# Optimization experiments

Hardware: AMD Instinct MI355X
Metric: run time of the kernel (lower is better)

Reference implementation:

```python
import jax, jax.numpy as jnp
import numpy as np

B, T_IN, F, H = 256, 168, 128, 512
T_OUT = 48


def setup_inputs() -> dict:
    key = jax.random.key(0)
    ks = jax.random.split(key, 8)
    s = 1.0 / np.sqrt(H)
    return {
        "x": jax.random.normal(ks[0], (B, T_IN, F), dtype=jnp.float32),
        "enc_Wih": jax.random.normal(ks[1], (4 * H, F), dtype=jnp.float32) * s,
        "enc_Whh": jax.random.normal(ks[2], (4 * H, H), dtype=jnp.float32) * s,
        "enc_b": jax.random.normal(ks[3], (4 * H,), dtype=jnp.float32) * s,
        "dec_Wih": jax.random.normal(ks[4], (4 * H, F), dtype=jnp.float32) * s,
        "dec_Whh": jax.random.normal(ks[5], (4 * H, H), dtype=jnp.float32) * s,
        "dec_b": jax.random.normal(ks[6], (4 * H,), dtype=jnp.float32) * s,
        "W_lin": jax.random.normal(ks[7], (F, H), dtype=jnp.float32) * s,
        "t_out": T_OUT,
    }


def _lstm_cell(h, c, xt, Wih, Whh, b):
    # torch gate order: i, f, g, o
    gates = xt @ Wih.T + h @ Whh.T + b  # [B, 4H]
    i, f, g, o = jnp.split(gates, 4, axis=-1)
    c_new = jax.nn.sigmoid(f) * c + jax.nn.sigmoid(i) * jnp.tanh(g)
    h_new = jax.nn.sigmoid(o) * jnp.tanh(c_new)
    return h_new, c_new


def reference(x, enc_Wih, enc_Whh, enc_b, dec_Wih, dec_Whh, dec_b, W_lin, t_out):
    bsz = x.shape[0]
    hidden = enc_Whh.shape[1]
    h0 = jnp.zeros((bsz, hidden), x.dtype)
    c0 = jnp.zeros((bsz, hidden), x.dtype)

    # ---- encoder: scan over T_in ----
    def enc_step(carry, xt):
        h, c = carry
        h, c = _lstm_cell(h, c, xt, enc_Wih, enc_Whh, enc_b)
        return (h, c), None

    (hn, cn), _ = jax.lax.scan(enc_step, (h0, c0), jnp.swapaxes(x, 0, 1))

    # ---- decoder: recursive feeding, scan over T_out ----
    dec_in0 = x[:, -1, :]  # [B, F]

    def dec_step(carry, _):
        h, c, inp = carry
        h, c = _lstm_cell(h, c, inp, dec_Wih, dec_Whh, dec_b)
        out = h @ W_lin.T  # [B, F]
        return (h, c, out), out

    _, outs = jax.lax.scan(dec_step, (hn, cn, dec_in0), None, length=t_out)
    return jnp.swapaxes(outs, 0, 1)  # [B, T_out, F]
```

## Files before the change

kernel.cpp:

```cpp
#include <hip/hip_runtime.h>
#include <hip/hip_bf16.h>

typedef __bf16 bf16_t;
typedef __bf16 bf16x8 __attribute__((ext_vector_type(8)));
typedef __bf16 bf16x4 __attribute__((ext_vector_type(4)));
typedef float  f32x4  __attribute__((ext_vector_type(4)));
typedef unsigned int u32;
typedef unsigned long long u64;

#define HID 512
#define BATCH 256
#define TIN 168
#define TOUT 48
#define FEAT 128
#define NSTEPS (TIN + TOUT)
#define NGRP 8
#define NJT 32
#define GRPB 32

__device__ __forceinline__ float sigmoidf_(float x) {
    x = fminf(fmaxf(x, -30.f), 30.f);
    return 1.f / (1.f + __expf(-x));
}
__device__ __forceinline__ float tanhf_(float x) {
    x = fminf(fmaxf(x, -15.f), 15.f);
    float e = __expf(2.f * x);
    return (e - 1.f) / (e + 1.f);
}

__device__ __forceinline__ bf16x8 ld_h8(const bf16_t* p) {
    union { u64 q[2]; bf16x8 v; } u;
    u.q[0] = __hip_atomic_load((const u64*)p,     __ATOMIC_RELAXED,
                               __HIP_MEMORY_SCOPE_SYSTEM);
    u.q[1] = __hip_atomic_load((const u64*)p + 1, __ATOMIC_RELAXED,
                               __HIP_MEMORY_SCOPE_SYSTEM);
    return u.v;
}
__device__ __forceinline__ void st_h4(bf16_t* p, float v0, float v1, float v2, float v3) {
    bf16_t b0 = (bf16_t)v0, b1 = (bf16_t)v1, b2 = (bf16_t)v2, b3 = (bf16_t)v3;
    unsigned short s0, s1, s2, s3;
    __builtin_memcpy(&s0, &b0, 2); __builtin_memcpy(&s1, &b1, 2);
    __builtin_memcpy(&s2, &b2, 2); __builtin_memcpy(&s3, &b3, 2);
    u64 w = (u64)s0 | ((u64)s1 << 16) | ((u64)s2 << 32) | ((u64)s3 << 48);
    __hip_atomic_store((u64*)p, w, __ATOMIC_RELAXED, __HIP_MEMORY_SCOPE_SYSTEM);
}

__global__ __launch_bounds__(256)
void cast_x_kernel(const float* __restrict__ x, bf16_t* __restrict__ Xbf) {
    int q = blockIdx.x * 256 + threadIdx.x;
    if (q >= BATCH * TIN * (FEAT / 4)) return;
    int f4  = q & 31;
    int rem = q >> 5;
    int t = rem % TIN;
    int b = rem / TIN;
    float4 v = *(const float4*)&x[((size_t)b * TIN + t) * FEAT + f4 * 4];
    bf16x4 o = { (bf16_t)v.x, (bf16_t)v.y, (bf16_t)v.z, (bf16_t)v.w };
    *(bf16x4*)&Xbf[((size_t)t * BATCH + b) * FEAT + f4 * 4] = o;
}

__global__ __launch_bounds__(256)
void cast_wcat_kernel(const float* __restrict__ Wih, const float* __restrict__ Whh,
                      bf16_t* __restrict__ Wcat) {
    int q = blockIdx.x * 256 + threadIdx.x;
    int k4 = q % 160;
    int r  = q / 160;
    if (r >= 2048) return;
    int k = k4 * 4;
    float4 v;
    if (k < FEAT) v = *(const float4*)&Wih[(size_t)r * FEAT + k];
    else          v = *(const float4*)&Whh[(size_t)r * HID + (k - FEAT)];
    bf16x4 o = { (bf16_t)v.x, (bf16_t)v.y, (bf16_t)v.z, (bf16_t)v.w };
    *(bf16x4*)&Wcat[(size_t)r * 640 + k] = o;
}

__global__ __launch_bounds__(256)
void cast_wlin_kernel(const float* __restrict__ W, bf16_t* __restrict__ Wb) {
    int q = blockIdx.x * 256 + threadIdx.x;
    if (q >= FEAT * HID / 4) return;
    float4 v = *(const float4*)&W[q * 4];
    bf16x4 o = { (bf16_t)v.x, (bf16_t)v.y, (bf16_t)v.z, (bf16_t)v.w };
    *(bf16x4*)&Wb[q * 4] = o;
}

__global__ __launch_bounds__(256)
void build_wcomb_kernel(const float* __restrict__ dWih, const float* __restrict__ dWhh,
                        const float* __restrict__ Wlin, bf16_t* __restrict__ Wcomb) {
    __shared__ float As[64][128];
    __shared__ float Bs[128][64];
    int r0 = blockIdx.x * 64, c0 = blockIdx.y * 64;
    int tid = threadIdx.x;
    for (int i = tid; i < 64 * 32; i += 256) {
        int rr = i >> 5, cc = (i & 31) << 2;
        *(float4*)&As[rr][cc] = *(const float4*)&dWih[(size_t)(r0 + rr) * 128 + cc];
    }
    for (int i = tid; i < 128 * 16; i += 256) {
        int kk = i >> 4, cc = (i & 15) << 2;
        *(float4*)&Bs[kk][cc] = *(const float4*)&Wlin[(size_t)kk * HID + c0 + cc];
    }
    __syncthreads();
    int tx = tid & 15, ty = tid >> 4;
    float acc[4][4] = {};
    for (int k = 0; k < 128; ++k) {
        float a[4], b[4];
        #pragma unroll
        for (int i = 0; i < 4; ++i) a[i] = As[ty * 4 + i][k];
        #pragma unroll
        for (int j = 0; j < 4; ++j) b[j] = Bs[k][tx * 4 + j];
        #pragma unroll
        for (int i = 0; i < 4; ++i)
            #pragma unroll
            for (int j = 0; j < 4; ++j) acc[i][j] += a[i] * b[j];
    }
    for (int i = 0; i < 4; ++i) {
        int r = r0 + ty * 4 + i;
        for (int j = 0; j < 4; ++j) {
            int cc = c0 + tx * 4 + j;
            Wcomb[(size_t)r * HID + cc] = (bf16_t)(acc[i][j] + dWhh[(size_t)r * HID + cc]);
        }
    }
}


__device__ __forceinline__ void group_wait(const u32* flags, int g, int tid,
                                           unsigned int epoch) {
    if (tid < NJT) {
        while (__hip_atomic_load(&flags[g * NJT + tid], __ATOMIC_RELAXED,
                                 __HIP_MEMORY_SCOPE_SYSTEM) < epoch)
            __builtin_amdgcn_s_sleep(1);
    }
    __syncthreads();
}

__device__ __forceinline__ void group_arrive(u32* flags, int g, int jt, int tid,
                                             unsigned int epoch) {
    if (tid == 0)
        __hip_atomic_store(&flags[g * NJT + jt], epoch, __ATOMIC_RELAXED,
                           __HIP_MEMORY_SCOPE_SYSTEM);
}

__device__ __forceinline__ void cell_finish(
    f32x4 (&acc)[4], float (&cacc)[4], f32x4 (*Ex)[2][64],
    int gp, int bh, int lane, int l15, int l4, int brow, int jq0,
    bf16_t* __restrict__ hnext)
{
    if (gp == 1) {
        #pragma unroll
        for (int q = 0; q < 4; ++q)
            Ex[q][bh][lane] = acc[q];
    }
    __syncthreads();
    if (gp == 0) {
        #pragma unroll
        for (int q = 0; q < 4; ++q)
            acc[q] += Ex[q][bh][lane];
        float hv[4];
        #pragma unroll
        for (int r = 0; r < 4; ++r) {
            float cn = sigmoidf_(acc[1][r]) * cacc[r] + sigmoidf_(acc[0][r]) * tanhf_(acc[2][r]);
            cacc[r] = cn;
            hv[r] = sigmoidf_(acc[3][r]) * tanhf_(cn);
        }
        st_h4(hnext + (size_t)brow * HID + jq0, hv[0], hv[1], hv[2], hv[3]);
        asm volatile("s_waitcnt vmcnt(0)" ::: "memory");
    }
    __syncthreads();
}

__global__ __launch_bounds__(256, 1)
void lstm_persist(const bf16_t* __restrict__ Xbf,
                  const bf16_t* __restrict__ Wenc, const float* __restrict__ enc_b,
                  const bf16_t* __restrict__ Wdec1, const bf16_t* __restrict__ Wcomb,
                  const float* __restrict__ dec_b,
                  bf16_t* __restrict__ hbufA, bf16_t* __restrict__ hbufB,
                  bf16_t* __restrict__ Hdec, u32* __restrict__ flags)
{
    __shared__ f32x4 Ex[4][2][64];
    const int bid = blockIdx.x;
    const int g   = bid & (NGRP - 1);
    const int jt  = bid >> 3;
    const int j0  = jt * 16;
    const int tid = threadIdx.x;
    const int wave = tid >> 6, lane = tid & 63;
    const int l15 = lane & 15, l4 = lane >> 4;
    const int bh = wave & 1, gp = wave >> 1;
    const int b0 = g * GRPB + bh * 16;
    const int arow = b0 + l15;
    const int jcol = j0 + l15;
    const int jq0  = j0 + l4 * 4;

    f32x4 biasE4[4], biasD4[4];
    #pragma unroll
    for (int q = 0; q < 4; ++q) {
        biasE4[q] = *(const f32x4*)&enc_b[q * HID + jq0];
        biasD4[q] = *(const f32x4*)&dec_b[q * HID + jq0];
    }
    float cacc[4] = {0.f, 0.f, 0.f, 0.f};

    bf16x8 Breg[40];
    const int kc0 = gp * 320;

    #pragma unroll
    for (int q = 0; q < 4; ++q)
        #pragma unroll
        for (int i = 0; i < 10; ++i)
            Breg[q * 10 + i] = *(const bf16x8*)(
                Wenc + (size_t)(q * HID + jcol) * 640 + kc0 + i * 32 + l4 * 8);
    #pragma unroll
    for (int n = 0; n < 40; ++n) asm volatile("" : "+v"(Breg[n]));

    for (int t = 0; t < TIN; ++t) {
        if (t > 0) group_wait(flags, g, tid, (unsigned)t);
        const bf16_t* hb = (t & 1) ? hbufB : hbufA;
        bf16_t* hn       = (t & 1) ? hbufA : hbufB;
        const bf16_t* xb  = Xbf + ((size_t)t * BATCH + arow) * FEAT + l4 * 8;
        const bf16_t* hbp = hb + (size_t)arow * HID + l4 * 8;
        bf16x8 a[10];
        if (gp == 0) {
            #pragma unroll
            for (int i = 0; i < 4; ++i)  a[i] = *(const bf16x8*)(xb + i * 32);
            #pragma unroll
            for (int i = 4; i < 10; ++i) a[i] = ld_h8(hbp + (i * 32 - FEAT));
        } else {
            #pragma unroll
            for (int i = 0; i < 10; ++i) a[i] = ld_h8(hbp + (320 - FEAT) + i * 32);
        }
        f32x4 acc[4];
        #pragma unroll
        for (int q = 0; q < 4; ++q)
            acc[q] = (gp == 0) ? biasE4[q] : (f32x4){0.f, 0.f, 0.f, 0.f};
        #pragma unroll
        for (int i = 0; i < 10; ++i)
            #pragma unroll
            for (int q = 0; q < 4; ++q)
                acc[q] = __builtin_amdgcn_mfma_f32_16x16x32_bf16(Breg[q * 10 + i], a[i], acc[q], 0, 0, 0);
        cell_finish(acc, cacc, Ex, gp, bh, lane, l15, l4, arow, jq0, hn);
        group_arrive(flags, g, jt, tid, (unsigned)(t + 1));
    }

    #pragma unroll
    for (int q = 0; q < 4; ++q)
        #pragma unroll
        for (int i = 0; i < 10; ++i)
            Breg[q * 10 + i] = *(const bf16x8*)(
                Wdec1 + (size_t)(q * HID + jcol) * 640 + kc0 + i * 32 + l4 * 8);
    #pragma unroll
    for (int n = 0; n < 40; ++n) asm volatile("" : "+v"(Breg[n]));

    {
        const int t = TIN;
        group_wait(flags, g, tid, (unsigned)t);
        const bf16_t* xb  = Xbf + ((size_t)(TIN - 1) * BATCH + arow) * FEAT + l4 * 8;
        const bf16_t* hbp = hbufA + (size_t)arow * HID + l4 * 8;
        bf16x8 a[10];
        if (gp == 0) {
            #pragma unroll
            for (int i = 0; i < 4; ++i)  a[i] = *(const bf16x8*)(xb + i * 32);
            #pragma unroll
            for (int i = 4; i < 10; ++i) a[i] = ld_h8(hbp + (i * 32 - FEAT));
        } else {
            #pragma unroll
            for (int i = 0; i < 10; ++i) a[i] = ld_h8(hbp + (320 - FEAT) + i * 32);
        }
        f32x4 acc[4];
        #pragma unroll
        for (int q = 0; q < 4; ++q)
            acc[q] = (gp == 0) ? biasD4[q] : (f32x4){0.f, 0.f, 0.f, 0.f};
        #pragma unroll
        for (int i = 0; i < 10; ++i)
            #pragma unroll
            for (int q = 0; q < 4; ++q)
                acc[q] = __builtin_amdgcn_mfma_f32_16x16x32_bf16(Breg[q * 10 + i], a[i], acc[q], 0, 0, 0);
        cell_finish(acc, cacc, Ex, gp, bh, lane, l15, l4, arow, jq0, Hdec);
        group_arrive(flags, g, jt, tid, (unsigned)(t + 1));
    }

    const int kd0 = gp * 256;
    #pragma unroll
    for (int q = 0; q < 4; ++q)
        #pragma unroll
        for (int i = 0; i < 8; ++i)
            Breg[q * 8 + i] = *(const bf16x8*)(
                Wcomb + (size_t)(q * HID + jcol) * HID + kd0 + i * 32 + l4 * 8);
    #pragma unroll
    for (int n = 0; n < 32; ++n) asm volatile("" : "+v"(Breg[n]));

    for (int t = TIN + 1; t < NSTEPS; ++t) {
        group_wait(flags, g, tid, (unsigned)t);
        const bf16_t* hprev = Hdec + (size_t)(t - 1 - TIN) * BATCH * HID
                                   + (size_t)arow * HID + l4 * 8;
        bf16x8 a[8];
        #pragma unroll
        for (int i = 0; i < 8; ++i)
            a[i] = ld_h8(hprev + kd0 + i * 32);
        f32x4 acc[4];
        #pragma unroll
        for (int q = 0; q < 4; ++q)
            acc[q] = (gp == 0) ? biasD4[q] : (f32x4){0.f, 0.f, 0.f, 0.f};
        #pragma unroll
        for (int i = 0; i < 8; ++i)
            #pragma unroll
            for (int q = 0; q < 4; ++q)
                acc[q] = __builtin_amdgcn_mfma_f32_16x16x32_bf16(Breg[q * 8 + i], a[i], acc[q], 0, 0, 0);
        cell_finish(acc, cacc, Ex, gp, bh, lane, l15, l4, arow, jq0,
                    Hdec + (size_t)(t - TIN) * BATCH * HID);
        group_arrive(flags, g, jt, tid, (unsigned)(t + 1));
    }
}

__global__ __launch_bounds__(128)
void final_proj_kernel(const bf16_t* __restrict__ Hdec, const bf16_t* __restrict__ Wlin,
                       float* __restrict__ out) {
    int tid = threadIdx.x;
    int wv = tid >> 6, lane = tid & 63;
    int l15 = lane & 15, l4 = lane >> 4;
    int row0 = blockIdx.x * 32 + wv * 16;
    const bf16_t* arow = Hdec + (size_t)(row0 + l15) * HID;
    f32x4 acc[8];
    #pragma unroll
    for (int n = 0; n < 8; ++n) acc[n] = (f32x4){0.f, 0.f, 0.f, 0.f};
    #pragma unroll 4
    for (int kc = 0; kc < HID; kc += 32) {
        bf16x8 af = *(const bf16x8*)(arow + kc + l4 * 8);
        #pragma unroll
        for (int n = 0; n < 8; ++n) {
            bf16x8 bfr = *(const bf16x8*)(Wlin + (size_t)(n * 16 + l15) * HID + kc + l4 * 8);
            acc[n] = __builtin_amdgcn_mfma_f32_16x16x32_bf16(af, bfr, acc[n], 0, 0, 0);
        }
    }
    #pragma unroll
    for (int n = 0; n < 8; ++n) {
        int f = n * 16 + l15;
        #pragma unroll
        for (int r = 0; r < 4; ++r) {
            int row = row0 + l4 * 4 + r;
            int t = row >> 8;
            int b = row & 255;
            out[(size_t)b * (TOUT * FEAT) + (size_t)t * FEAT + f] = acc[n][r];
        }
    }
}

extern "C" void kernel_launch(void* const* d_in, const int* in_sizes, int n_in,
                              void* d_out, int out_size, void* d_ws, size_t ws_size,
                              hipStream_t stream) {
    const float* x       = (const float*)d_in[0];
    const float* enc_Wih = (const float*)d_in[1];
    const float* enc_Whh = (const float*)d_in[2];
    const float* enc_b   = (const float*)d_in[3];
    const float* dec_Wih = (const float*)d_in[4];
    const float* dec_Whh = (const float*)d_in[5];
    const float* dec_b   = (const float*)d_in[6];
    const float* W_lin   = (const float*)d_in[7];
    float* out = (float*)d_out;

    char* p = (char*)d_ws;
    auto alloc = [&](size_t bytes) -> void* {
        void* r = (void*)p;
        p += (bytes + 255) & ~(size_t)255;
        return r;
    };
    bf16_t* Xbf    = (bf16_t*)alloc((size_t)TIN * BATCH * FEAT * 2);
    bf16_t* Wenc   = (bf16_t*)alloc((size_t)2048 * 640 * 2);
    bf16_t* Wdec1  = (bf16_t*)alloc((size_t)2048 * 640 * 2);
    bf16_t* Wcomb  = (bf16_t*)alloc((size_t)2048 * HID * 2);
    bf16_t* Wlinb  = (bf16_t*)alloc((size_t)FEAT * HID * 2);
    bf16_t* hbufA  = (bf16_t*)alloc((size_t)BATCH * HID * 2);
    bf16_t* hbufB  = (bf16_t*)alloc((size_t)BATCH * HID * 2);
    bf16_t* Hdec   = (bf16_t*)alloc((size_t)TOUT * BATCH * HID * 2);
    u32* flags     = (u32*)alloc((size_t)NGRP * NJT * 4);

    (void)hipMemsetAsync(hbufA, 0, (size_t)BATCH * HID * 2, stream);
    (void)hipMemsetAsync(flags, 0, (size_t)NGRP * NJT * 4, stream);

    cast_x_kernel<<<(BATCH * TIN * (FEAT / 4) + 255) / 256, 256, 0, stream>>>(x, Xbf);
    cast_wcat_kernel<<<(2048 * 160 + 255) / 256, 256, 0, stream>>>(enc_Wih, enc_Whh, Wenc);
    cast_wcat_kernel<<<(2048 * 160 + 255) / 256, 256, 0, stream>>>(dec_Wih, dec_Whh, Wdec1);
    cast_wlin_kernel<<<(FEAT * HID / 4 + 255) / 256, 256, 0, stream>>>(W_lin, Wlinb);
    build_wcomb_kernel<<<dim3(2048 / 64, HID / 64), 256, 0, stream>>>(dec_Wih, dec_Whh, W_lin, Wcomb);

    lstm_persist<<<NGRP * NJT, 256, 0, stream>>>(Xbf, Wenc, enc_b, Wdec1, Wcomb, dec_b,
                                                 hbufA, hbufB, Hdec, flags);

    final_proj_kernel<<<(TOUT * BATCH) / 32, 128, 0, stream>>>(Hdec, Wlinb, out);
}
```

Measured before the change: 1.004 ms.

## Replace block-wide barrier sync with per-wave dependency flags in persistent LSTM

```diff
diff --git a/kernel.cpp b/kernel.cpp
--- a/kernel.cpp
+++ b/kernel.cpp
@@ -121,49 +121,36 @@
 }
 
 
-__device__ __forceinline__ void group_wait(const u32* flags, int g, int tid,
-                                           unsigned int epoch) {
-    if (tid < NJT) {
-        while (__hip_atomic_load(&flags[g * NJT + tid], __ATOMIC_RELAXED,
+__device__ __forceinline__ void wave_wait(const u32* flags, int g, int bh,
+                                          int jt0, int nf, int lane, u32 epoch) {
+    if (lane < nf) {
+        const u32* fp = &flags[g * 64 + (jt0 + lane) * 2 + bh];
+        while (__hip_atomic_load(fp, __ATOMIC_RELAXED,
                                  __HIP_MEMORY_SCOPE_SYSTEM) < epoch)
             __builtin_amdgcn_s_sleep(1);
     }
-    __syncthreads();
-}
-
-__device__ __forceinline__ void group_arrive(u32* flags, int g, int jt, int tid,
-                                             unsigned int epoch) {
-    if (tid == 0)
-        __hip_atomic_store(&flags[g * NJT + jt], epoch, __ATOMIC_RELAXED,
-                           __HIP_MEMORY_SCOPE_SYSTEM);
-}
-
-__device__ __forceinline__ void cell_finish(
-    f32x4 (&acc)[4], float (&cacc)[4], f32x4 (*Ex)[2][64],
-    int gp, int bh, int lane, int l15, int l4, int brow, int jq0,
-    bf16_t* __restrict__ hnext)
+}
+
+__device__ __forceinline__ void cell_store(
+    f32x4 (&acc)[4], float (&cacc)[4], const f32x4 (*Exp)[2][64],
+    u32* flags, int g, int jt, int bh, int lane, int brow, int jq0,
+    u32 epoch_next, bf16_t* __restrict__ hnext)
 {
-    if (gp == 1) {
-        #pragma unroll
-        for (int q = 0; q < 4; ++q)
-            Ex[q][bh][lane] = acc[q];
-    }
-    __syncthreads();
-    if (gp == 0) {
-        #pragma unroll
-        for (int q = 0; q < 4; ++q)
-            acc[q] += Ex[q][bh][lane];
-        float hv[4];
-        #pragma unroll
-        for (int r = 0; r < 4; ++r) {
-            float cn = sigmoidf_(acc[1][r]) * cacc[r] + sigmoidf_(acc[0][r]) * tanhf_(acc[2][r]);
-            cacc[r] = cn;
-            hv[r] = sigmoidf_(acc[3][r]) * tanhf_(cn);
-        }
-        st_h4(hnext + (size_t)brow * HID + jq0, hv[0], hv[1], hv[2], hv[3]);
-        asm volatile("s_waitcnt vmcnt(0)" ::: "memory");
-    }
-    __syncthreads();
+    #pragma unroll
+    for (int q = 0; q < 4; ++q)
+        acc[q] += Exp[q][bh][lane];
+    float hv[4];
+    #pragma unroll
+    for (int r = 0; r < 4; ++r) {
+        float cn = sigmoidf_(acc[1][r]) * cacc[r] + sigmoidf_(acc[0][r]) * tanhf_(acc[2][r]);
+        cacc[r] = cn;
+        hv[r] = sigmoidf_(acc[3][r]) * tanhf_(cn);
+    }
+    st_h4(hnext + (size_t)brow * HID + jq0, hv[0], hv[1], hv[2], hv[3]);
+    asm volatile("s_waitcnt vmcnt(0)" ::: "memory");
+    if (lane == 0)
+        __hip_atomic_store(&flags[g * 64 + jt * 2 + bh], epoch_next,
+                           __ATOMIC_RELAXED, __HIP_MEMORY_SCOPE_SYSTEM);
 }
 
 __global__ __launch_bounds__(256, 1)
@@ -174,7 +161,7 @@
                   bf16_t* __restrict__ hbufA, bf16_t* __restrict__ hbufB,
                   bf16_t* __restrict__ Hdec, u32* __restrict__ flags)
 {
-    __shared__ f32x4 Ex[4][2][64];
+    __shared__ f32x4 Ex[2][4][2][64];
     const int bid = blockIdx.x;
     const int g   = bid & (NGRP - 1);
     const int jt  = bid >> 3;
@@ -198,6 +185,8 @@
 
     bf16x8 Breg[40];
     const int kc0 = gp * 320;
+    const int encJt0 = gp ? 12 : 0;
+    const int encNf  = gp ? 20 : 12;
 
     #pragma unroll
     for (int q = 0; q < 4; ++q)
@@ -209,15 +198,18 @@
     for (int n = 0; n < 40; ++n) asm volatile("" : "+v"(Breg[n]));
 
     for (int t = 0; t < TIN; ++t) {
-        if (t > 0) group_wait(flags, g, tid, (unsigned)t);
+        const int par = t & 1;
         const bf16_t* hb = (t & 1) ? hbufB : hbufA;
         bf16_t* hn       = (t & 1) ? hbufA : hbufB;
-        const bf16_t* xb  = Xbf + ((size_t)t * BATCH + arow) * FEAT + l4 * 8;
+        bf16x8 a[10];
+        const bf16_t* xb = Xbf + ((size_t)t * BATCH + arow) * FEAT + l4 * 8;
+        if (gp == 0) {
+            #pragma unroll
+            for (int i = 0; i < 4; ++i) a[i] = *(const bf16x8*)(xb + i * 32);
+        }
+        if (t > 0) wave_wait(flags, g, bh, encJt0, encNf, lane, (u32)t);
         const bf16_t* hbp = hb + (size_t)arow * HID + l4 * 8;
-        bf16x8 a[10];
         if (gp == 0) {
-            #pragma unroll
-            for (int i = 0; i < 4; ++i)  a[i] = *(const bf16x8*)(xb + i * 32);
             #pragma unroll
             for (int i = 4; i < 10; ++i) a[i] = ld_h8(hbp + (i * 32 - FEAT));
         } else {
@@ -233,8 +225,15 @@
             #pragma unroll
             for (int q = 0; q < 4; ++q)
                 acc[q] = __builtin_amdgcn_mfma_f32_16x16x32_bf16(Breg[q * 10 + i], a[i], acc[q], 0, 0, 0);
-        cell_finish(acc, cacc, Ex, gp, bh, lane, l15, l4, arow, jq0, hn);
-        group_arrive(flags, g, jt, tid, (unsigned)(t + 1));
+        if (gp == 1) {
+            #pragma unroll
+            for (int q = 0; q < 4; ++q)
+                Ex[par][q][bh][lane] = acc[q];
+        }
+        __syncthreads();
+        if (gp == 0)
+            cell_store(acc, cacc, Ex[par], flags, g, jt, bh, lane, arow, jq0,
+                       (u32)(t + 1), hn);
     }
 
     #pragma unroll
@@ -248,13 +247,16 @@
 
     {
         const int t = TIN;
-        group_wait(flags, g, tid, (unsigned)t);
-        const bf16_t* xb  = Xbf + ((size_t)(TIN - 1) * BATCH + arow) * FEAT + l4 * 8;
+        const int par = t & 1;
+        bf16x8 a[10];
+        const bf16_t* xb = Xbf + ((size_t)(TIN - 1) * BATCH + arow) * FEAT + l4 * 8;
+        if (gp == 0) {
+            #pragma unroll
+            for (int i = 0; i < 4; ++i) a[i] = *(const bf16x8*)(xb + i * 32);
+        }
+        wave_wait(flags, g, bh, encJt0, encNf, lane, (u32)t);
         const bf16_t* hbp = hbufA + (size_t)arow * HID + l4 * 8;
-        bf16x8 a[10];
         if (gp == 0) {
-            #pragma unroll
-            for (int i = 0; i < 4; ++i)  a[i] = *(const bf16x8*)(xb + i * 32);
             #pragma unroll
             for (int i = 4; i < 10; ++i) a[i] = ld_h8(hbp + (i * 32 - FEAT));
         } else {
@@ -270,11 +272,19 @@
             #pragma unroll
             for (int q = 0; q < 4; ++q)
                 acc[q] = __builtin_amdgcn_mfma_f32_16x16x32_bf16(Breg[q * 10 + i], a[i], acc[q], 0, 0, 0);
-        cell_finish(acc, cacc, Ex, gp, bh, lane, l15, l4, arow, jq0, Hdec);
-        group_arrive(flags, g, jt, tid, (unsigned)(t + 1));
+        if (gp == 1) {
+            #pragma unroll
+            for (int q = 0; q < 4; ++q)
+                Ex[par][q][bh][lane] = acc[q];
+        }
+        __syncthreads();
+        if (gp == 0)
+            cell_store(acc, cacc, Ex[par], flags, g, jt, bh, lane, arow, jq0,
+                       (u32)(t + 1), Hdec);
     }
 
     const int kd0 = gp * 256;
+    const int decJt0 = gp ? 16 : 0;
     #pragma unroll
     for (int q = 0; q < 4; ++q)
         #pragma unroll
@@ -285,7 +295,8 @@
     for (int n = 0; n < 32; ++n) asm volatile("" : "+v"(Breg[n]));
 
     for (int t = TIN + 1; t < NSTEPS; ++t) {
-        group_wait(flags, g, tid, (unsigned)t);
+        const int par = t & 1;
+        wave_wait(flags, g, bh, decJt0, 16, lane, (u32)t);
         const bf16_t* hprev = Hdec + (size_t)(t - 1 - TIN) * BATCH * HID
                                    + (size_t)arow * HID + l4 * 8;
         bf16x8 a[8];
@@ -301,9 +312,15 @@
             #pragma unroll
             for (int q = 0; q < 4; ++q)
                 acc[q] = __builtin_amdgcn_mfma_f32_16x16x32_bf16(Breg[q * 8 + i], a[i], acc[q], 0, 0, 0);
-        cell_finish(acc, cacc, Ex, gp, bh, lane, l15, l4, arow, jq0,
-                    Hdec + (size_t)(t - TIN) * BATCH * HID);
-        group_arrive(flags, g, jt, tid, (unsigned)(t + 1));
+        if (gp == 1) {
+            #pragma unroll
+            for (int q = 0; q < 4; ++q)
+                Ex[par][q][bh][lane] = acc[q];
+        }
+        __syncthreads();
+        if (gp == 0)
+            cell_store(acc, cacc, Ex[par], flags, g, jt, bh, lane, arow, jq0,
+                       (u32)(t + 1), Hdec + (size_t)(t - TIN) * BATCH * HID);
     }
 }
 
@@ -367,10 +384,10 @@
     bf16_t* hbufA  = (bf16_t*)alloc((size_t)BATCH * HID * 2);
     bf16_t* hbufB  = (bf16_t*)alloc((size_t)BATCH * HID * 2);
     bf16_t* Hdec   = (bf16_t*)alloc((size_t)TOUT * BATCH * HID * 2);
-    u32* flags     = (u32*)alloc((size_t)NGRP * NJT * 4);
+    u32* flags     = (u32*)alloc((size_t)NGRP * 64 * 4);
 
     (void)hipMemsetAsync(hbufA, 0, (size_t)BATCH * HID * 2, stream);
-    (void)hipMemsetAsync(flags, 0, (size_t)NGRP * NJT * 4, stream);
+    (void)hipMemsetAsync(flags, 0, (size_t)NGRP * 64 * 4, stream);
 
     cast_x_kernel<<<(BATCH * TIN * (FEAT / 4) + 255) / 256, 256, 0, stream>>>(x, Xbf);
     cast_wcat_kernel<<<(2048 * 160 + 255) / 256, 256, 0, stream>>>(enc_Wih, enc_Whh, Wenc);
```

After: 1.869 ms, median of 2. 86.2% more time.

## Double per-block hidden-column width to halve cross-block flag synchronization

Applied to the files above, without the earlier changes.

```diff
diff --git a/kernel.cpp b/kernel.cpp
--- a/kernel.cpp
+++ b/kernel.cpp
@@ -15,7 +15,7 @@
 #define FEAT 128
 #define NSTEPS (TIN + TOUT)
 #define NGRP 8
-#define NJT 32
+#define NJT 16
 #define GRPB 32
 
 __device__ __forceinline__ float sigmoidf_(float x) {
@@ -122,7 +122,7 @@
 
 
 __device__ __forceinline__ void group_wait(const u32* flags, int g, int tid,
-                                           unsigned int epoch) {
+                                           u32 epoch) {
     if (tid < NJT) {
         while (__hip_atomic_load(&flags[g * NJT + tid], __ATOMIC_RELAXED,
                                  __HIP_MEMORY_SCOPE_SYSTEM) < epoch)
@@ -132,27 +132,27 @@
 }
 
 __device__ __forceinline__ void group_arrive(u32* flags, int g, int jt, int tid,
-                                             unsigned int epoch) {
+                                             u32 epoch) {
     if (tid == 0)
         __hip_atomic_store(&flags[g * NJT + jt], epoch, __ATOMIC_RELAXED,
                            __HIP_MEMORY_SCOPE_SYSTEM);
 }
 
 __device__ __forceinline__ void cell_finish(
-    f32x4 (&acc)[4], float (&cacc)[4], f32x4 (*Ex)[2][64],
-    int gp, int bh, int lane, int l15, int l4, int brow, int jq0,
+    f32x4 (&acc)[4], float (&cacc)[4], f32x4 (*Ex)[4][64],
+    int gp, int sub, int lane, int brow, int jq0,
     bf16_t* __restrict__ hnext)
 {
     if (gp == 1) {
         #pragma unroll
         for (int q = 0; q < 4; ++q)
-            Ex[q][bh][lane] = acc[q];
+            Ex[q][sub][lane] = acc[q];
     }
     __syncthreads();
     if (gp == 0) {
         #pragma unroll
         for (int q = 0; q < 4; ++q)
-            acc[q] += Ex[q][bh][lane];
+            acc[q] += Ex[q][sub][lane];
         float hv[4];
         #pragma unroll
         for (int r = 0; r < 4; ++r) {
@@ -166,7 +166,7 @@
     __syncthreads();
 }
 
-__global__ __launch_bounds__(256, 1)
+__global__ __launch_bounds__(512, 1)
 void lstm_persist(const bf16_t* __restrict__ Xbf,
                   const bf16_t* __restrict__ Wenc, const float* __restrict__ enc_b,
                   const bf16_t* __restrict__ Wdec1, const bf16_t* __restrict__ Wcomb,
@@ -174,19 +174,21 @@
                   bf16_t* __restrict__ hbufA, bf16_t* __restrict__ hbufB,
                   bf16_t* __restrict__ Hdec, u32* __restrict__ flags)
 {
-    __shared__ f32x4 Ex[4][2][64];
+    __shared__ f32x4 Ex[4][4][64];
     const int bid = blockIdx.x;
     const int g   = bid & (NGRP - 1);
     const int jt  = bid >> 3;
-    const int j0  = jt * 16;
+    const int j0  = jt * 32;
     const int tid = threadIdx.x;
     const int wave = tid >> 6, lane = tid & 63;
     const int l15 = lane & 15, l4 = lane >> 4;
-    const int bh = wave & 1, gp = wave >> 1;
+    const int ch = wave & 1, bh = (wave >> 1) & 1, gp = wave >> 2;
+    const int sub = bh * 2 + ch;
+    const int jbase = j0 + ch * 16;
     const int b0 = g * GRPB + bh * 16;
     const int arow = b0 + l15;
-    const int jcol = j0 + l15;
-    const int jq0  = j0 + l4 * 4;
+    const int jcol = jbase + l15;
+    const int jq0  = jbase + l4 * 4;
 
     f32x4 biasE4[4], biasD4[4];
     #pragma unroll
@@ -209,7 +211,7 @@
     for (int n = 0; n < 40; ++n) asm volatile("" : "+v"(Breg[n]));
 
     for (int t = 0; t < TIN; ++t) {
-        if (t > 0) group_wait(flags, g, tid, (unsigned)t);
+        if (t > 0) group_wait(flags, g, tid, (u32)t);
         const bf16_t* hb = (t & 1) ? hbufB : hbufA;
         bf16_t* hn       = (t & 1) ? hbufA : hbufB;
         const bf16_t* xb  = Xbf + ((size_t)t * BATCH + arow) * FEAT + l4 * 8;
@@ -233,8 +235,8 @@
             #pragma unroll
             for (int q = 0; q < 4; ++q)
                 acc[q] = __builtin_amdgcn_mfma_f32_16x16x32_bf16(Breg[q * 10 + i], a[i], acc[q], 0, 0, 0);
-        cell_finish(acc, cacc, Ex, gp, bh, lane, l15, l4, arow, jq0, hn);
-        group_arrive(flags, g, jt, tid, (unsigned)(t + 1));
+        cell_finish(acc, cacc, Ex, gp, sub, lane, arow, jq0, hn);
+        group_arrive(flags, g, jt, tid, (u32)(t + 1));
     }
 
     #pragma unroll
@@ -248,7 +250,7 @@
 
     {
         const int t = TIN;
-        group_wait(flags, g, tid, (unsigned)t);
+        group_wait(flags, g, tid, (u32)t);
         const bf16_t* xb  = Xbf + ((size_t)(TIN - 1) * BATCH + arow) * FEAT + l4 * 8;
         const bf16_t* hbp = hbufA + (size_t)arow * HID + l4 * 8;
         bf16x8 a[10];
@@ -270,8 +272,8 @@
             #pragma unroll
             for (int q = 0; q < 4; ++q)
                 acc[q] = __builtin_amdgcn_mfma_f32_16x16x32_bf16(Breg[q * 10 + i], a[i], acc[q], 0, 0, 0);
-        cell_finish(acc, cacc, Ex, gp, bh, lane, l15, l4, arow, jq0, Hdec);
-        group_arrive(flags, g, jt, tid, (unsigned)(t + 1));
+        cell_finish(acc, cacc, Ex, gp, sub, lane, arow, jq0, Hdec);
+        group_arrive(flags, g, jt, tid, (u32)(t + 1));
     }
 
     const int kd0 = gp * 256;
@@ -285,7 +287,7 @@
     for (int n = 0; n < 32; ++n) asm volatile("" : "+v"(Breg[n]));
 
     for (int t = TIN + 1; t < NSTEPS; ++t) {
-        group_wait(flags, g, tid, (unsigned)t);
+        group_wait(flags, g, tid, (u32)t);
         const bf16_t* hprev = Hdec + (size_t)(t - 1 - TIN) * BATCH * HID
                                    + (size_t)arow * HID + l4 * 8;
         bf16x8 a[8];
@@ -301,9 +303,9 @@
             #pragma unroll
             for (int q = 0; q < 4; ++q)
                 acc[q] = __builtin_amdgcn_mfma_f32_16x16x32_bf16(Breg[q * 8 + i], a[i], acc[q], 0, 0, 0);
-        cell_finish(acc, cacc, Ex, gp, bh, lane, l15, l4, arow, jq0,
+        cell_finish(acc, cacc, Ex, gp, sub, lane, arow, jq0,
                     Hdec + (size_t)(t - TIN) * BATCH * HID);
-        group_arrive(flags, g, jt, tid, (unsigned)(t + 1));
+        group_arrive(flags, g, jt, tid, (u32)(t + 1));
     }
 }
 
@@ -378,7 +380,7 @@
     cast_wlin_kernel<<<(FEAT * HID / 4 + 255) / 256, 256, 0, stream>>>(W_lin, Wlinb);
     build_wcomb_kernel<<<dim3(2048 / 64, HID / 64), 256, 0, stream>>>(dec_Wih, dec_Whh, W_lin, Wcomb);
 
-    lstm_persist<<<NGRP * NJT, 256, 0, stream>>>(Xbf, Wenc, enc_b, Wdec1, Wcomb, dec_b,
+    lstm_persist<<<NGRP * NJT, 512, 0, stream>>>(Xbf, Wenc, enc_b, Wdec1, Wcomb, dec_b,
                                                  hbufA, hbufB, Hdec, flags);
 
     final_proj_kernel<<<(TOUT * BATCH) / 32, 128, 0, stream>>>(Hdec, Wlinb, out);
```

Measured after the change: 1.524 ms. 51.9% more time.
